# Kernel tuning notes

Measured on AMD Instinct MI355X. Metric: run time of the kernel, lower is better.

The kernel has to match this reference:

```python
import jax, jax.numpy as jnp
import numpy as np

N_NODES = 100000
N_EDGES = 1600000
D_IN = 32
D_OUT = 32
K_HOPS = 2
CUTGRAPH = 0.2
EPS = 1e-12  # torch F.normalize eps


def setup_inputs() -> dict:
    key = jax.random.key(0)
    k1, k2, k3, k4 = jax.random.split(key, 4)
    features = jax.random.normal(k1, (N_NODES, D_IN), dtype=jnp.float32)
    W = jax.random.normal(k2, (D_OUT, D_IN), dtype=jnp.float32) * (1.0 / np.sqrt(D_IN))
    src = jax.random.randint(k3, (N_EDGES,), 0, N_NODES, dtype=jnp.int64 if jax.config.jax_enable_x64 else jnp.int32)
    dst = jax.random.randint(k4, (N_EDGES,), 0, N_NODES, dtype=jnp.int64 if jax.config.jax_enable_x64 else jnp.int32)
    return {"features": features, "W": W, "src": src, "dst": dst}


def reference(features, W, src, dst):
    N = features.shape[0]
    E = src.shape[0]
    cut_k = int(E * CUTGRAPH)  # static edge count to prune

    # symmetric degree norm: deg^{-1/2} over in-degrees, clamped at 1
    deg = jax.ops.segment_sum(jnp.ones((E,), features.dtype), dst, num_segments=N)
    norm = jnp.power(jnp.clip(deg, 1.0, None), -0.5)[:, None]  # [N,1]

    h = features
    for _ in range(K_HOPS):
        # cosine-similarity edge pruning: zero the cut_k lowest-cos edges
        nrm = jnp.linalg.norm(h, axis=-1, keepdims=True)
        nh = h / jnp.maximum(nrm, EPS)  # F.normalize(p=2)
        cos = jnp.sum(nh[src] * nh[dst], axis=-1)  # [E]
        _, low_idx = jax.lax.top_k(-cos, cut_k)    # indices of smallest cos
        w = jnp.ones((E,), h.dtype).at[low_idx].set(0.0)

        h = h * norm
        msg = h[src] * w[:, None]                       # u_mul_e gather [E,D]
        h = jax.ops.segment_sum(msg, dst, num_segments=N)  # sum scatter
        h = h * norm

    return h @ W.T  # fc (bias=False)
```

## Files before the change

### kernel.cpp

```cpp
#include <hip/hip_runtime.h>
#include <hip/hip_bf16.h>
#include <stdint.h>

#define N_NODES 100000
#define N_EDGES 1600000
#define D_FEAT 32
#define CUT_K 320000
#define COSKEY_NB 4096
#define HC_NB 1000
#define HC_SLICE 1600
#define SCAN_NB ((N_NODES + 255) / 256)

struct SelState { unsigned long long prefix; unsigned int k; };

__global__ void deg_kernel(const int* __restrict__ dst, int* __restrict__ deg, int E) {
    int e = blockIdx.x * blockDim.x + threadIdx.x;
    if (e < E) atomicAdd(&deg[dst[e]], 1);
}

__global__ void norm_kernel(const int* __restrict__ deg, float* __restrict__ nrm, int N) {
    int i = blockIdx.x * blockDim.x + threadIdx.x;
    if (i < N) nrm[i] = 1.0f / sqrtf(fmaxf((float)deg[i], 1.0f));
}

__global__ void blocksum_kernel(const int* __restrict__ deg, int* __restrict__ bsum, int N) {
    int i = blockIdx.x * 256 + threadIdx.x;
    int v = (i < N) ? deg[i] : 0;
#pragma unroll
    for (int off = 32; off > 0; off >>= 1) v += __shfl_down(v, off, 64);
    __shared__ int ws4[4];
    if ((threadIdx.x & 63) == 0) ws4[threadIdx.x >> 6] = v;
    __syncthreads();
    if (threadIdx.x == 0) bsum[blockIdx.x] = ws4[0] + ws4[1] + ws4[2] + ws4[3];
}

__global__ void scanpartial_kernel(const int* __restrict__ bsum, int* __restrict__ boff, int B) {
    __shared__ int buf[512];
    int t = threadIdx.x;
    int v = (t < B) ? bsum[t] : 0;
    buf[t] = v;
    __syncthreads();
    for (int off = 1; off < 512; off <<= 1) {
        int u = (t >= off) ? buf[t - off] : 0;
        __syncthreads();
        buf[t] += u;
        __syncthreads();
    }
    if (t < B) boff[t] = buf[t] - v;
}

__global__ void writeoffs_kernel(const int* __restrict__ deg, const int* __restrict__ boff,
                                 int* __restrict__ offs, int* __restrict__ cursor, int N) {
    __shared__ int buf[256];
    int t = threadIdx.x;
    int i = blockIdx.x * 256 + t;
    int v = (i < N) ? deg[i] : 0;
    buf[t] = v;
    __syncthreads();
    for (int off = 1; off < 256; off <<= 1) {
        int u = (t >= off) ? buf[t - off] : 0;
        __syncthreads();
        buf[t] += u;
        __syncthreads();
    }
    int ex = buf[t] - v + boff[blockIdx.x];
    if (i < N) { offs[i] = ex; cursor[i] = ex; }
    if (i == N - 1) offs[N] = ex + v;
}

__global__ void fill_kernel(const int* __restrict__ src, const int* __restrict__ dst,
                            int* __restrict__ cursor,
                            int* __restrict__ csr_src, int* __restrict__ csr_dst,
                            int* __restrict__ csr_eid, int E) {
    int e = blockIdx.x * blockDim.x + threadIdx.x;
    if (e >= E) return;
    int d = dst[e];
    int pos = atomicAdd(&cursor[d], 1);
    csr_src[pos] = src[e];
    csr_dst[pos] = d;
    csr_eid[pos] = e;
}

__global__ void rownorm_kernel(const float* __restrict__ h, float* __restrict__ nh,
                               float* __restrict__ hs, const float* __restrict__ nrm,
                               SelState* __restrict__ st, int N) {
    int i = blockIdx.x * blockDim.x + threadIdx.x;
    if (i == 0) { st->prefix = 0ull; st->k = CUT_K; }
    if (i >= N) return;
    const float4* hp = (const float4*)(h + (size_t)i * D_FEAT);
    float4 v[8];
    float ss = 0.f;
#pragma unroll
    for (int q = 0; q < 8; ++q) {
        v[q] = hp[q];
        ss += v[q].x * v[q].x + v[q].y * v[q].y + v[q].z * v[q].z + v[q].w * v[q].w;
    }
    float inv = 1.0f / fmaxf(sqrtf(ss), 1e-12f);
    float sc = nrm[i];
    float4* op = (float4*)(nh + (size_t)i * D_FEAT);
    float4* sp = (float4*)(hs + (size_t)i * D_FEAT);
#pragma unroll
    for (int q = 0; q < 8; ++q) {
        float4 ov = v[q];
        float4 sv = v[q];
        ov.x *= inv; ov.y *= inv; ov.z *= inv; ov.w *= inv;
        sv.x *= sc;  sv.y *= sc;  sv.z *= sc;  sv.w *= sc;
        op[q] = ov;
        sp[q] = sv;
    }
}

__global__ void coskey_kernel(const float* __restrict__ nh, const int* __restrict__ csr_src,
                              const int* __restrict__ csr_dst, const int* __restrict__ csr_eid,
                              unsigned long long* __restrict__ keys,
                              unsigned int* __restrict__ ghist, int E) {
    __shared__ unsigned int lh[4][256];
    int t = threadIdx.x;
#pragma unroll
    for (int w = 0; w < 4; ++w) lh[w][t] = 0u;
    __syncthreads();
    int wave = t >> 6;
    int stride = gridDim.x * blockDim.x;
    for (int p = blockIdx.x * blockDim.x + t; p < E; p += stride) {
        const float4* a = (const float4*)(nh + (size_t)csr_src[p] * D_FEAT);
        const float4* b = (const float4*)(nh + (size_t)csr_dst[p] * D_FEAT);
        float s = 0.f;
#pragma unroll
        for (int q = 0; q < 8; ++q) {
            float4 x = a[q], y = b[q];
            s += x.x * y.x + x.y * y.y + x.z * y.z + x.w * y.w;
        }
        unsigned int u = __float_as_uint(s);
        unsigned int so = (u & 0x80000000u) ? ~u : (u | 0x80000000u);
        unsigned long long key = ((unsigned long long)so << 32) | (unsigned int)csr_eid[p];
        keys[p] = key;
        atomicAdd(&lh[wave][(unsigned int)(key >> 56)], 1u);
    }
    __syncthreads();
    unsigned int tot = lh[0][t] + lh[1][t] + lh[2][t] + lh[3][t];
    if (tot) atomicAdd(&ghist[t], tot);
}

__global__ void histc_kernel(const unsigned long long* __restrict__ in,
                             const int* __restrict__ cnt_in,
                             unsigned long long* __restrict__ out,
                             int* __restrict__ cnt_out,
                             const SelState* __restrict__ st,
                             unsigned int* __restrict__ ghist, int pass) {
    __shared__ unsigned int lh[4][256];
    __shared__ unsigned int lcnt;
    int t = threadIdx.x, b = blockIdx.x;
#pragma unroll
    for (int w = 0; w < 4; ++w) lh[w][t] = 0u;
    if (t == 0) lcnt = 0u;
    __syncthreads();
    unsigned long long prefix = st->prefix;
    int n = cnt_in ? cnt_in[b] : HC_SLICE;
    const unsigned long long* sin = in + (size_t)b * HC_SLICE;
    unsigned long long* sout = out + (size_t)b * HC_SLICE;
    int wave = t >> 6;
    int fshift = 64 - 8 * pass;
    int dshift = 56 - 8 * pass;
    for (int i = t; i < n; i += 256) {
        unsigned long long key = sin[i];
        if ((key >> fshift) == prefix) {
            atomicAdd(&lh[wave][(unsigned int)((key >> dshift) & 0xFFull)], 1u);
            unsigned int slot = atomicAdd(&lcnt, 1u);
            sout[slot] = key;
        }
    }
    __syncthreads();
    if (t == 0) cnt_out[b] = (int)lcnt;
    unsigned int tot = lh[0][t] + lh[1][t] + lh[2][t] + lh[3][t];
    if (tot) atomicAdd(&ghist[t], tot);
}

__global__ void scan8_kernel(unsigned int* __restrict__ ghist, SelState* __restrict__ st) {
    __shared__ unsigned int buf[256];
    int t = threadIdx.x;
    unsigned int k = st->k;
    unsigned int s = ghist[t];
    buf[t] = s;
    __syncthreads();
    for (int off = 1; off < 256; off <<= 1) {
        unsigned int v = (t >= off) ? buf[t - off] : 0u;
        __syncthreads();
        buf[t] += v;
        __syncthreads();
    }
    unsigned int incl = buf[t];
    unsigned int excl = incl - s;
    if (excl < k && k <= incl) {
        st->prefix = (st->prefix << 8) | (unsigned long long)t;
        st->k = k - excl;
    }
    ghist[t] = 0u;
}

__global__ void aggregate_csr_kernel(const float* __restrict__ hs, float* __restrict__ h_out,
                                     const int* __restrict__ offs, const int* __restrict__ csr_src,
                                     const unsigned long long* __restrict__ keys,
                                     const SelState* __restrict__ st,
                                     const float* __restrict__ nrm, int N) {
    unsigned long long kth = st->prefix;
    int g = blockIdx.x * 8 + (threadIdx.x >> 5);
    int j = threadIdx.x & 31;
    if (g >= N) return;
    int lo = offs[g], hi = offs[g + 1];
    float acc = 0.f;
    int p = lo;
    for (; p + 8 <= hi; p += 8) {
        unsigned long long kk[8];
        int ss[8];
#pragma unroll
        for (int u = 0; u < 8; ++u) { kk[u] = keys[p + u]; ss[u] = csr_src[p + u]; }
        float vv[8];
#pragma unroll
        for (int u = 0; u < 8; ++u) vv[u] = hs[(size_t)ss[u] * D_FEAT + j];
#pragma unroll
        for (int u = 0; u < 8; ++u) acc += (kk[u] > kth) ? vv[u] : 0.f;
    }
    for (; p < hi; ++p) {
        if (keys[p] > kth) acc += hs[(size_t)csr_src[p] * D_FEAT + j];
    }
    h_out[(size_t)g * D_FEAT + j] = acc * nrm[g];
}

__global__ void fc_kernel(const float* __restrict__ h, const float* __restrict__ W,
                          float* __restrict__ out, int N) {
    __shared__ float Wt[32][33];
    int t = threadIdx.x;
    for (int i = t; i < 1024; i += 256) Wt[i & 31][i >> 5] = W[i];
    __syncthreads();
    int node = blockIdx.x * 8 + (t >> 5);
    if (node >= N) return;
    int o = t & 31;
    const float* hr = h + (size_t)node * D_FEAT;
    float acc = 0.f;
#pragma unroll
    for (int j = 0; j < 32; ++j) acc += hr[j] * Wt[j][o];
    out[(size_t)node * D_FEAT + o] = acc;
}

extern "C" void kernel_launch(void* const* d_in, const int* in_sizes, int n_in,
                              void* d_out, int out_size, void* d_ws, size_t ws_size,
                              hipStream_t stream) {
    const float* features = (const float*)d_in[0];
    const float* W        = (const float*)d_in[1];
    const int*   src      = (const int*)d_in[2];
    const int*   dst      = (const int*)d_in[3];
    float*       out      = (float*)d_out;

    char* ws = (char*)d_ws;
    size_t o = 0;
    auto take = [&](size_t bytes) -> char* {
        char* p = ws + o;
        o += (bytes + 255) & ~(size_t)255;
        return p;
    };
    int*                deg     = (int*)take((size_t)N_NODES * 4);
    float*              nrm     = (float*)take((size_t)N_NODES * 4);
    int*                offs    = (int*)take((size_t)(N_NODES + 1) * 4);
    int*                cursor  = (int*)take((size_t)N_NODES * 4);
    int*                csr_src = (int*)take((size_t)N_EDGES * 4);
    int*                csr_dst = (int*)take((size_t)N_EDGES * 4);
    int*                csr_eid = (int*)take((size_t)N_EDGES * 4);
    float*              hA      = (float*)take((size_t)N_NODES * D_FEAT * 4);
    float*              hB      = (float*)take((size_t)N_NODES * D_FEAT * 4);
    float*              nh      = (float*)take((size_t)N_NODES * D_FEAT * 4);
    float*              hs      = (float*)take((size_t)N_NODES * D_FEAT * 4);
    unsigned long long* keys    = (unsigned long long*)take((size_t)N_EDGES * 8);
    unsigned int*       ghist   = (unsigned int*)take((size_t)256 * 4);
    SelState*           st      = (SelState*)take(256);
    int*                bsum    = (int*)take((size_t)SCAN_NB * 4);
    int*                boff    = (int*)take((size_t)SCAN_NB * 4);
    int*                cnt_a   = (int*)take((size_t)HC_NB * 4);
    int*                cnt_b   = (int*)take((size_t)HC_NB * 4);

    unsigned long long* candA = (unsigned long long*)nh;
    unsigned long long* candB = (unsigned long long*)hB;

    hipMemsetAsync(deg, 0, (size_t)N_NODES * 4, stream);
    hipMemsetAsync(ghist, 0, (size_t)256 * 4, stream);

    deg_kernel<<<(N_EDGES + 255) / 256, 256, 0, stream>>>(dst, deg, N_EDGES);
    norm_kernel<<<(N_NODES + 255) / 256, 256, 0, stream>>>(deg, nrm, N_NODES);
    blocksum_kernel<<<SCAN_NB, 256, 0, stream>>>(deg, bsum, N_NODES);
    scanpartial_kernel<<<1, 512, 0, stream>>>(bsum, boff, SCAN_NB);
    writeoffs_kernel<<<SCAN_NB, 256, 0, stream>>>(deg, boff, offs, cursor, N_NODES);
    fill_kernel<<<(N_EDGES + 255) / 256, 256, 0, stream>>>(src, dst, cursor,
                                                           csr_src, csr_dst, csr_eid, N_EDGES);

    const float* hin = features;
    float* houts[2] = { hA, hB };
    for (int hop = 0; hop < 2; ++hop) {
        float* hout = houts[hop];
        rownorm_kernel<<<(N_NODES + 255) / 256, 256, 0, stream>>>(hin, nh, hs, nrm, st, N_NODES);
        coskey_kernel<<<COSKEY_NB, 256, 0, stream>>>(nh, csr_src, csr_dst, csr_eid,
                                                     keys, ghist, N_EDGES);
        scan8_kernel<<<1, 256, 0, stream>>>(ghist, st);
        for (int pass = 1; pass < 8; ++pass) {
            const unsigned long long* in =
                (pass == 1) ? keys : ((pass & 1) ? candB : candA);
            const int* cin = (pass == 1) ? (const int*)nullptr
                                         : ((pass & 1) ? cnt_b : cnt_a);
            unsigned long long* outc = (pass & 1) ? candA : candB;
            int* cout = (pass & 1) ? cnt_a : cnt_b;
            histc_kernel<<<HC_NB, 256, 0, stream>>>(in, cin, outc, cout, st, ghist, pass);
            scan8_kernel<<<1, 256, 0, stream>>>(ghist, st);
        }
        aggregate_csr_kernel<<<(N_NODES + 7) / 8, 256, 0, stream>>>(
            hs, hout, offs, csr_src, keys, st, nrm, N_NODES);
        hin = hout;
    }
    fc_kernel<<<(N_NODES + 7) / 8, 256, 0, stream>>>(hin, W, out, N_NODES);
}
```

Measured before the change: 632.8 us.

## Pack CSR src and edge id into one word, walk coskey per destination

Merges csr_src and csr_eid into one 64-bit array and drops csr_dst. The cosine-key kernel now assigns 32 lanes to each destination node, loads that node's normalized row once into registers and loops over its incoming edges, instead of gathering both endpoint rows for every edge. The fill kernel processes four edges per thread. This cuts one row gather per edge and one index stream, in exchange for an imbalanced per-node loop, a 1-to-8-byte index read in aggregation, and more register use.

Measured after the change: 863.4 us. 1.36x slower.

```diff
diff --git a/kernel.cpp b/kernel.cpp
--- a/kernel.cpp
+++ b/kernel.cpp
@@ -6,7 +6,6 @@
 #define N_EDGES 1600000
 #define D_FEAT 32
 #define CUT_K 320000
-#define COSKEY_NB 4096
 #define HC_NB 1000
 #define HC_SLICE 1600
 #define SCAN_NB ((N_NODES + 255) / 256)
@@ -70,15 +69,17 @@
 
 __global__ void fill_kernel(const int* __restrict__ src, const int* __restrict__ dst,
                             int* __restrict__ cursor,
-                            int* __restrict__ csr_src, int* __restrict__ csr_dst,
-                            int* __restrict__ csr_eid, int E) {
-    int e = blockIdx.x * blockDim.x + threadIdx.x;
-    if (e >= E) return;
-    int d = dst[e];
-    int pos = atomicAdd(&cursor[d], 1);
-    csr_src[pos] = src[e];
-    csr_dst[pos] = d;
-    csr_eid[pos] = e;
+                            unsigned long long* __restrict__ csr_se, int E) {
+    int e0 = blockIdx.x * 1024 + threadIdx.x;
+#pragma unroll
+    for (int u = 0; u < 4; ++u) {
+        int e = e0 + u * 256;
+        if (e < E) {
+            int d = dst[e];
+            int pos = atomicAdd(&cursor[d], 1);
+            csr_se[pos] = ((unsigned long long)(unsigned int)src[e] << 32) | (unsigned int)e;
+        }
+    }
 }
 
 __global__ void rownorm_kernel(const float* __restrict__ h, float* __restrict__ nh,
@@ -110,31 +111,39 @@
     }
 }
 
-__global__ void coskey_kernel(const float* __restrict__ nh, const int* __restrict__ csr_src,
-                              const int* __restrict__ csr_dst, const int* __restrict__ csr_eid,
+__global__ void coskey_kernel(const float* __restrict__ nh, const int* __restrict__ offs,
+                              const unsigned long long* __restrict__ csr_se,
                               unsigned long long* __restrict__ keys,
-                              unsigned int* __restrict__ ghist, int E) {
+                              unsigned int* __restrict__ ghist, int N) {
     __shared__ unsigned int lh[4][256];
     int t = threadIdx.x;
 #pragma unroll
     for (int w = 0; w < 4; ++w) lh[w][t] = 0u;
     __syncthreads();
     int wave = t >> 6;
-    int stride = gridDim.x * blockDim.x;
-    for (int p = blockIdx.x * blockDim.x + t; p < E; p += stride) {
-        const float4* a = (const float4*)(nh + (size_t)csr_src[p] * D_FEAT);
-        const float4* b = (const float4*)(nh + (size_t)csr_dst[p] * D_FEAT);
-        float s = 0.f;
-#pragma unroll
-        for (int q = 0; q < 8; ++q) {
-            float4 x = a[q], y = b[q];
-            s += x.x * y.x + x.y * y.y + x.z * y.z + x.w * y.w;
+    int g = blockIdx.x * 8 + (t >> 5);
+    int j = t & 31;
+    if (g < N) {
+        const float4* bp = (const float4*)(nh + (size_t)g * D_FEAT);
+        float4 bv[8];
+#pragma unroll
+        for (int q = 0; q < 8; ++q) bv[q] = bp[q];
+        int lo = offs[g], hi = offs[g + 1];
+        for (int p = lo + j; p < hi; p += 32) {
+            unsigned long long pk = csr_se[p];
+            const float4* ap = (const float4*)(nh + (size_t)(pk >> 32) * D_FEAT);
+            float s = 0.f;
+#pragma unroll
+            for (int q = 0; q < 8; ++q) {
+                float4 x = ap[q];
+                s += x.x * bv[q].x + x.y * bv[q].y + x.z * bv[q].z + x.w * bv[q].w;
+            }
+            unsigned int u = __float_as_uint(s);
+            unsigned int so = (u & 0x80000000u) ? ~u : (u | 0x80000000u);
+            unsigned long long key = ((unsigned long long)so << 32) | (unsigned int)pk;
+            keys[p] = key;
+            atomicAdd(&lh[wave][(unsigned int)(key >> 56)], 1u);
         }
-        unsigned int u = __float_as_uint(s);
-        unsigned int so = (u & 0x80000000u) ? ~u : (u | 0x80000000u);
-        unsigned long long key = ((unsigned long long)so << 32) | (unsigned int)csr_eid[p];
-        keys[p] = key;
-        atomicAdd(&lh[wave][(unsigned int)(key >> 56)], 1u);
     }
     __syncthreads();
     unsigned int tot = lh[0][t] + lh[1][t] + lh[2][t] + lh[3][t];
@@ -198,7 +207,8 @@
 }
 
 __global__ void aggregate_csr_kernel(const float* __restrict__ hs, float* __restrict__ h_out,
-                                     const int* __restrict__ offs, const int* __restrict__ csr_src,
+                                     const int* __restrict__ offs,
+                                     const unsigned long long* __restrict__ csr_se,
                                      const unsigned long long* __restrict__ keys,
                                      const SelState* __restrict__ st,
                                      const float* __restrict__ nrm, int N) {
@@ -210,18 +220,17 @@
     float acc = 0.f;
     int p = lo;
     for (; p + 8 <= hi; p += 8) {
-        unsigned long long kk[8];
-        int ss[8];
-#pragma unroll
-        for (int u = 0; u < 8; ++u) { kk[u] = keys[p + u]; ss[u] = csr_src[p + u]; }
+        unsigned long long kk[8], se[8];
+#pragma unroll
+        for (int u = 0; u < 8; ++u) { kk[u] = keys[p + u]; se[u] = csr_se[p + u]; }
         float vv[8];
 #pragma unroll
-        for (int u = 0; u < 8; ++u) vv[u] = hs[(size_t)ss[u] * D_FEAT + j];
+        for (int u = 0; u < 8; ++u) vv[u] = hs[(size_t)(se[u] >> 32) * D_FEAT + j];
 #pragma unroll
         for (int u = 0; u < 8; ++u) acc += (kk[u] > kth) ? vv[u] : 0.f;
     }
     for (; p < hi; ++p) {
-        if (keys[p] > kth) acc += hs[(size_t)csr_src[p] * D_FEAT + j];
+        if (keys[p] > kth) acc += hs[(size_t)(csr_se[p] >> 32) * D_FEAT + j];
     }
     h_out[(size_t)g * D_FEAT + j] = acc * nrm[g];
 }
@@ -262,9 +271,7 @@
     float*              nrm     = (float*)take((size_t)N_NODES * 4);
     int*                offs    = (int*)take((size_t)(N_NODES + 1) * 4);
     int*                cursor  = (int*)take((size_t)N_NODES * 4);
-    int*                csr_src = (int*)take((size_t)N_EDGES * 4);
-    int*                csr_dst = (int*)take((size_t)N_EDGES * 4);
-    int*                csr_eid = (int*)take((size_t)N_EDGES * 4);
+    unsigned long long* csr_se  = (unsigned long long*)take((size_t)N_EDGES * 8);
     float*              hA      = (float*)take((size_t)N_NODES * D_FEAT * 4);
     float*              hB      = (float*)take((size_t)N_NODES * D_FEAT * 4);
     float*              nh      = (float*)take((size_t)N_NODES * D_FEAT * 4);
@@ -288,16 +295,16 @@
     blocksum_kernel<<<SCAN_NB, 256, 0, stream>>>(deg, bsum, N_NODES);
     scanpartial_kernel<<<1, 512, 0, stream>>>(bsum, boff, SCAN_NB);
     writeoffs_kernel<<<SCAN_NB, 256, 0, stream>>>(deg, boff, offs, cursor, N_NODES);
-    fill_kernel<<<(N_EDGES + 255) / 256, 256, 0, stream>>>(src, dst, cursor,
-                                                           csr_src, csr_dst, csr_eid, N_EDGES);
+    fill_kernel<<<(N_EDGES + 1023) / 1024, 256, 0, stream>>>(src, dst, cursor,
+                                                             csr_se, N_EDGES);
 
     const float* hin = features;
     float* houts[2] = { hA, hB };
     for (int hop = 0; hop < 2; ++hop) {
         float* hout = houts[hop];
         rownorm_kernel<<<(N_NODES + 255) / 256, 256, 0, stream>>>(hin, nh, hs, nrm, st, N_NODES);
-        coskey_kernel<<<COSKEY_NB, 256, 0, stream>>>(nh, csr_src, csr_dst, csr_eid,
-                                                     keys, ghist, N_EDGES);
+        coskey_kernel<<<(N_NODES + 7) / 8, 256, 0, stream>>>(nh, offs, csr_se,
+                                                             keys, ghist, N_NODES);
         scan8_kernel<<<1, 256, 0, stream>>>(ghist, st);
         for (int pass = 1; pass < 8; ++pass) {
             const unsigned long long* in =
@@ -310,7 +317,7 @@
             scan8_kernel<<<1, 256, 0, stream>>>(ghist, st);
         }
         aggregate_csr_kernel<<<(N_NODES + 7) / 8, 256, 0, stream>>>(
-            hs, hout, offs, csr_src, keys, st, nrm, N_NODES);
+            hs, hout, offs, csr_se, keys, st, nrm, N_NODES);
         hin = hout;
     }
     fc_kernel<<<(N_NODES + 7) / 8, 256, 0, stream>>>(hin, W, out, N_NODES);
```

## Fuse radix-select scan into last block and pack CSR into uint4

Applied to the files above, without the earlier changes.

Removes the separate single-block scan8 launches (16 per run) by having the last block of each coskey/histc kernel, detected via an atomic done-counter, perform the prefix scan and selection update. The separate csr_src/csr_dst/csr_eid arrays are also packed into one 16-byte uint4 record per edge, so coskey does one vector load instead of three. This cuts launch and dependency overhead but adds threadfence and atomics, and aggregate now reads 16-byte records to obtain only the source index, which wastes bandwidth.

Result: slower. 2.338 ms (+269.4%).

```diff
diff --git a/kernel.cpp b/kernel.cpp
--- a/kernel.cpp
+++ b/kernel.cpp
@@ -70,15 +70,18 @@
 
 __global__ void fill_kernel(const int* __restrict__ src, const int* __restrict__ dst,
                             int* __restrict__ cursor,
-                            int* __restrict__ csr_src, int* __restrict__ csr_dst,
-                            int* __restrict__ csr_eid, int E) {
-    int e = blockIdx.x * blockDim.x + threadIdx.x;
-    if (e >= E) return;
-    int d = dst[e];
-    int pos = atomicAdd(&cursor[d], 1);
-    csr_src[pos] = src[e];
-    csr_dst[pos] = d;
-    csr_eid[pos] = e;
+                            uint4* __restrict__ csr, int E) {
+    int e0 = blockIdx.x * 1024 + threadIdx.x;
+#pragma unroll
+    for (int u = 0; u < 4; ++u) {
+        int e = e0 + u * 256;
+        if (e < E) {
+            int d = dst[e];
+            int pos = atomicAdd(&cursor[d], 1);
+            csr[pos] = make_uint4((unsigned int)src[e], (unsigned int)d,
+                                  (unsigned int)e, 0u);
+        }
+    }
 }
 
 __global__ void rownorm_kernel(const float* __restrict__ h, float* __restrict__ nh,
@@ -110,11 +113,37 @@
     }
 }
 
-__global__ void coskey_kernel(const float* __restrict__ nh, const int* __restrict__ csr_src,
-                              const int* __restrict__ csr_dst, const int* __restrict__ csr_eid,
+__device__ __forceinline__ void block_select(unsigned int* ghist, SelState* st,
+                                             unsigned int* done) {
+    __shared__ unsigned int buf[256];
+    int t = threadIdx.x;
+    unsigned int k = st->k;
+    unsigned int s = atomicAdd(&ghist[t], 0u);
+    buf[t] = s;
+    __syncthreads();
+    for (int off = 1; off < 256; off <<= 1) {
+        unsigned int v = (t >= off) ? buf[t - off] : 0u;
+        __syncthreads();
+        buf[t] += v;
+        __syncthreads();
+    }
+    unsigned int incl = buf[t];
+    unsigned int excl = incl - s;
+    if (excl < k && k <= incl) {
+        st->prefix = (st->prefix << 8) | (unsigned long long)t;
+        st->k = k - excl;
+    }
+    ghist[t] = 0u;
+    if (t == 0) *done = 0u;
+}
+
+__global__ void coskey_kernel(const float* __restrict__ nh, const uint4* __restrict__ csr,
                               unsigned long long* __restrict__ keys,
-                              unsigned int* __restrict__ ghist, int E) {
+                              unsigned int* __restrict__ ghist,
+                              SelState* __restrict__ st,
+                              unsigned int* __restrict__ done, int E) {
     __shared__ unsigned int lh[4][256];
+    __shared__ unsigned int isLast;
     int t = threadIdx.x;
 #pragma unroll
     for (int w = 0; w < 4; ++w) lh[w][t] = 0u;
@@ -122,8 +151,9 @@
     int wave = t >> 6;
     int stride = gridDim.x * blockDim.x;
     for (int p = blockIdx.x * blockDim.x + t; p < E; p += stride) {
-        const float4* a = (const float4*)(nh + (size_t)csr_src[p] * D_FEAT);
-        const float4* b = (const float4*)(nh + (size_t)csr_dst[p] * D_FEAT);
+        uint4 r = csr[p];
+        const float4* a = (const float4*)(nh + (size_t)r.x * D_FEAT);
+        const float4* b = (const float4*)(nh + (size_t)r.y * D_FEAT);
         float s = 0.f;
 #pragma unroll
         for (int q = 0; q < 8; ++q) {
@@ -132,23 +162,29 @@
         }
         unsigned int u = __float_as_uint(s);
         unsigned int so = (u & 0x80000000u) ? ~u : (u | 0x80000000u);
-        unsigned long long key = ((unsigned long long)so << 32) | (unsigned int)csr_eid[p];
+        unsigned long long key = ((unsigned long long)so << 32) | r.z;
         keys[p] = key;
         atomicAdd(&lh[wave][(unsigned int)(key >> 56)], 1u);
     }
     __syncthreads();
     unsigned int tot = lh[0][t] + lh[1][t] + lh[2][t] + lh[3][t];
     if (tot) atomicAdd(&ghist[t], tot);
+    __threadfence();
+    if (t == 0) isLast = (atomicAdd(done, 1u) == gridDim.x - 1) ? 1u : 0u;
+    __syncthreads();
+    if (isLast) block_select(ghist, st, done);
 }
 
 __global__ void histc_kernel(const unsigned long long* __restrict__ in,
                              const int* __restrict__ cnt_in,
                              unsigned long long* __restrict__ out,
                              int* __restrict__ cnt_out,
-                             const SelState* __restrict__ st,
-                             unsigned int* __restrict__ ghist, int pass) {
+                             SelState* __restrict__ st,
+                             unsigned int* __restrict__ ghist,
+                             unsigned int* __restrict__ done, int pass) {
     __shared__ unsigned int lh[4][256];
     __shared__ unsigned int lcnt;
+    __shared__ unsigned int isLast;
     int t = threadIdx.x, b = blockIdx.x;
 #pragma unroll
     for (int w = 0; w < 4; ++w) lh[w][t] = 0u;
@@ -173,32 +209,15 @@
     if (t == 0) cnt_out[b] = (int)lcnt;
     unsigned int tot = lh[0][t] + lh[1][t] + lh[2][t] + lh[3][t];
     if (tot) atomicAdd(&ghist[t], tot);
-}
-
-__global__ void scan8_kernel(unsigned int* __restrict__ ghist, SelState* __restrict__ st) {
-    __shared__ unsigned int buf[256];
-    int t = threadIdx.x;
-    unsigned int k = st->k;
-    unsigned int s = ghist[t];
-    buf[t] = s;
-    __syncthreads();
-    for (int off = 1; off < 256; off <<= 1) {
-        unsigned int v = (t >= off) ? buf[t - off] : 0u;
-        __syncthreads();
-        buf[t] += v;
-        __syncthreads();
-    }
-    unsigned int incl = buf[t];
-    unsigned int excl = incl - s;
-    if (excl < k && k <= incl) {
-        st->prefix = (st->prefix << 8) | (unsigned long long)t;
-        st->k = k - excl;
-    }
-    ghist[t] = 0u;
+    __threadfence();
+    if (t == 0) isLast = (atomicAdd(done, 1u) == gridDim.x - 1) ? 1u : 0u;
+    __syncthreads();
+    if (isLast) block_select(ghist, st, done);
 }
 
 __global__ void aggregate_csr_kernel(const float* __restrict__ hs, float* __restrict__ h_out,
-                                     const int* __restrict__ offs, const int* __restrict__ csr_src,
+                                     const int* __restrict__ offs,
+                                     const uint4* __restrict__ csr,
                                      const unsigned long long* __restrict__ keys,
                                      const SelState* __restrict__ st,
                                      const float* __restrict__ nrm, int N) {
@@ -211,9 +230,9 @@
     int p = lo;
     for (; p + 8 <= hi; p += 8) {
         unsigned long long kk[8];
-        int ss[8];
-#pragma unroll
-        for (int u = 0; u < 8; ++u) { kk[u] = keys[p + u]; ss[u] = csr_src[p + u]; }
+        unsigned int ss[8];
+#pragma unroll
+        for (int u = 0; u < 8; ++u) { kk[u] = keys[p + u]; ss[u] = csr[p + u].x; }
         float vv[8];
 #pragma unroll
         for (int u = 0; u < 8; ++u) vv[u] = hs[(size_t)ss[u] * D_FEAT + j];
@@ -221,7 +240,7 @@
         for (int u = 0; u < 8; ++u) acc += (kk[u] > kth) ? vv[u] : 0.f;
     }
     for (; p < hi; ++p) {
-        if (keys[p] > kth) acc += hs[(size_t)csr_src[p] * D_FEAT + j];
+        if (keys[p] > kth) acc += hs[(size_t)csr[p].x * D_FEAT + j];
     }
     h_out[(size_t)g * D_FEAT + j] = acc * nrm[g];
 }
@@ -262,9 +281,7 @@
     float*              nrm     = (float*)take((size_t)N_NODES * 4);
     int*                offs    = (int*)take((size_t)(N_NODES + 1) * 4);
     int*                cursor  = (int*)take((size_t)N_NODES * 4);
-    int*                csr_src = (int*)take((size_t)N_EDGES * 4);
-    int*                csr_dst = (int*)take((size_t)N_EDGES * 4);
-    int*                csr_eid = (int*)take((size_t)N_EDGES * 4);
+    uint4*              csr     = (uint4*)take((size_t)N_EDGES * 16);
     float*              hA      = (float*)take((size_t)N_NODES * D_FEAT * 4);
     float*              hB      = (float*)take((size_t)N_NODES * D_FEAT * 4);
     float*              nh      = (float*)take((size_t)N_NODES * D_FEAT * 4);
@@ -272,6 +289,7 @@
     unsigned long long* keys    = (unsigned long long*)take((size_t)N_EDGES * 8);
     unsigned int*       ghist   = (unsigned int*)take((size_t)256 * 4);
     SelState*           st      = (SelState*)take(256);
+    unsigned int*       done    = (unsigned int*)take(256);
     int*                bsum    = (int*)take((size_t)SCAN_NB * 4);
     int*                boff    = (int*)take((size_t)SCAN_NB * 4);
     int*                cnt_a   = (int*)take((size_t)HC_NB * 4);
@@ -282,23 +300,22 @@
 
     hipMemsetAsync(deg, 0, (size_t)N_NODES * 4, stream);
     hipMemsetAsync(ghist, 0, (size_t)256 * 4, stream);
+    hipMemsetAsync(done, 0, 4, stream);
 
     deg_kernel<<<(N_EDGES + 255) / 256, 256, 0, stream>>>(dst, deg, N_EDGES);
     norm_kernel<<<(N_NODES + 255) / 256, 256, 0, stream>>>(deg, nrm, N_NODES);
     blocksum_kernel<<<SCAN_NB, 256, 0, stream>>>(deg, bsum, N_NODES);
     scanpartial_kernel<<<1, 512, 0, stream>>>(bsum, boff, SCAN_NB);
     writeoffs_kernel<<<SCAN_NB, 256, 0, stream>>>(deg, boff, offs, cursor, N_NODES);
-    fill_kernel<<<(N_EDGES + 255) / 256, 256, 0, stream>>>(src, dst, cursor,
-                                                           csr_src, csr_dst, csr_eid, N_EDGES);
+    fill_kernel<<<(N_EDGES + 1023) / 1024, 256, 0, stream>>>(src, dst, cursor,
+                                                             csr, N_EDGES);
 
     const float* hin = features;
     float* houts[2] = { hA, hB };
     for (int hop = 0; hop < 2; ++hop) {
         float* hout = houts[hop];
         rownorm_kernel<<<(N_NODES + 255) / 256, 256, 0, stream>>>(hin, nh, hs, nrm, st, N_NODES);
-        coskey_kernel<<<COSKEY_NB, 256, 0, stream>>>(nh, csr_src, csr_dst, csr_eid,
-                                                     keys, ghist, N_EDGES);
-        scan8_kernel<<<1, 256, 0, stream>>>(ghist, st);
+        coskey_kernel<<<COSKEY_NB, 256, 0, stream>>>(nh, csr, keys, ghist, st, done, N_EDGES);
         for (int pass = 1; pass < 8; ++pass) {
             const unsigned long long* in =
                 (pass == 1) ? keys : ((pass & 1) ? candB : candA);
@@ -306,11 +323,10 @@
                                          : ((pass & 1) ? cnt_b : cnt_a);
             unsigned long long* outc = (pass & 1) ? candA : candB;
             int* cout = (pass & 1) ? cnt_a : cnt_b;
-            histc_kernel<<<HC_NB, 256, 0, stream>>>(in, cin, outc, cout, st, ghist, pass);
-            scan8_kernel<<<1, 256, 0, stream>>>(ghist, st);
+            histc_kernel<<<HC_NB, 256, 0, stream>>>(in, cin, outc, cout, st, ghist, done, pass);
         }
         aggregate_csr_kernel<<<(N_NODES + 7) / 8, 256, 0, stream>>>(
-            hs, hout, offs, csr_src, keys, st, nrm, N_NODES);
+            hs, hout, offs, csr, keys, st, nrm, N_NODES);
         hin = hout;
     }
     fc_kernel<<<(N_NODES + 7) / 8, 256, 0, stream>>>(hin, W, out, N_NODES);
```
